# Kernel optimization log

Hardware: AMD Instinct MI355X
Metric: run time of the kernel (lower is better)

## Reference

```python
import jax, jax.numpy as jnp
import numpy as np

ENC_DIM = 128
DEC_DIM = 128
NUM_HEADS = 4
HEAD_DIM = DEC_DIM // NUM_HEADS


def _layernorm(x, g, b, eps=1e-5):
    mu = jnp.mean(x, axis=-1, keepdims=True)
    var = jnp.mean((x - mu) ** 2, axis=-1, keepdims=True)
    return (x - mu) * jax.lax.rsqrt(var + eps) * g + b


def setup_inputs() -> dict:
    key = jax.random.key(0)
    ks = jax.random.split(key, 12)
    B, H, W, D = 2, 16, 16, 16
    s = 0.02
    return {
        "encoder_feat": jax.random.normal(ks[0], (B, ENC_DIM, H, W, D), jnp.float32),
        "decoder_feat": jax.random.normal(ks[1], (B, DEC_DIM, H, W, D), jnp.float32),
        # torch Linear weights stored as [out, in]
        "Wq": jax.random.normal(ks[2], (DEC_DIM, DEC_DIM), jnp.float32) * s,
        "bq": jnp.zeros((DEC_DIM,), jnp.float32),
        "Wk": jax.random.normal(ks[3], (DEC_DIM, ENC_DIM), jnp.float32) * s,
        "bk": jnp.zeros((DEC_DIM,), jnp.float32),
        "Wv": jax.random.normal(ks[4], (DEC_DIM, ENC_DIM), jnp.float32) * s,
        "bv": jnp.zeros((DEC_DIM,), jnp.float32),
        "Wo": jax.random.normal(ks[5], (DEC_DIM, DEC_DIM), jnp.float32) * s,
        "bo": jnp.zeros((DEC_DIM,), jnp.float32),
        "g_enc": jnp.ones((ENC_DIM,), jnp.float32),
        "b_enc": jnp.zeros((ENC_DIM,), jnp.float32),
        "g_dec": jnp.ones((DEC_DIM,), jnp.float32),
        "b_dec": jnp.zeros((DEC_DIM,), jnp.float32),
        "g_out": jnp.ones((DEC_DIM,), jnp.float32),
        "b_out": jnp.zeros((DEC_DIM,), jnp.float32),
        "W1": jax.random.normal(ks[6], (DEC_DIM * 4, DEC_DIM), jnp.float32) * s,
        "b1": jnp.zeros((DEC_DIM * 4,), jnp.float32),
        "W2": jax.random.normal(ks[7], (DEC_DIM, DEC_DIM * 4), jnp.float32) * s,
        "b2": jnp.zeros((DEC_DIM,), jnp.float32),
    }


def reference(encoder_feat, decoder_feat, Wq, bq, Wk, bk, Wv, bv, Wo, bo,
              g_enc, b_enc, g_dec, b_dec, g_out, b_out, W1, b1, W2, b2):
    B, C_dec, H, W_, D = decoder_feat.shape
    N = H * W_ * D
    scale = HEAD_DIM ** -0.5
    # [B, C, H, W, D] -> [B, N, C]
    enc_seq = encoder_feat.reshape(B, -1, N).transpose(0, 2, 1)
    dec_seq = decoder_feat.reshape(B, C_dec, N).transpose(0, 2, 1)
    enc_seq = _layernorm(enc_seq, g_enc, b_enc)
    dec_seq = _layernorm(dec_seq, g_dec, b_dec)
    # projections (torch Linear: x @ W.T + b), split heads -> [B, h, N, d]
    Q = (dec_seq @ Wq.T + bq).reshape(B, N, NUM_HEADS, HEAD_DIM).transpose(0, 2, 1, 3)
    K = (enc_seq @ Wk.T + bk).reshape(B, N, NUM_HEADS, HEAD_DIM).transpose(0, 2, 1, 3)
    V = (enc_seq @ Wv.T + bv).reshape(B, N, NUM_HEADS, HEAD_DIM).transpose(0, 2, 1, 3)
    attn = jnp.einsum('bhqd,bhkd->bhqk', Q, K) * scale  # [B, h, N, N]
    attn = jax.nn.softmax(attn, axis=-1)
    out = jnp.einsum('bhqk,bhkd->bhqd', attn, V)
    out = out.transpose(0, 2, 1, 3).reshape(B, N, C_dec)
    out = out @ Wo.T + bo
    out = dec_seq + out
    h = _layernorm(out, g_out, b_out)
    ffn = jax.nn.gelu(h @ W1.T + b1, approximate=False) @ W2.T + b2
    out = out + ffn
    return out.transpose(0, 2, 1).reshape(B, C_dec, H, W_, D)
```

## Files before the change

kernel.cpp:

```cpp
#include <hip/hip_runtime.h>
#include <hip/hip_bf16.h>
#include <math.h>

#define B_ 2
#define N_ 4096
#define BN_ 8192
#define NH_ 4
#define SPLIT_ 8

using bf16x8   = __attribute__((ext_vector_type(8))) __bf16;
using f32x4    = __attribute__((ext_vector_type(4))) float;
using ushortx8 = __attribute__((ext_vector_type(8))) unsigned short;

#if __has_builtin(__builtin_amdgcn_exp2f)
#define FAST_EXP2(x) __builtin_amdgcn_exp2f(x)
#else
#define FAST_EXP2(x) __expf((x) * 0.6931471805599453f)
#endif

static __device__ __forceinline__ unsigned short f2bf(float f) {
    union { __hip_bfloat16 h; unsigned short u; } c;
    c.h = __float2bfloat16(f);
    return c.u;
}
static __device__ __forceinline__ float bf2f(unsigned short u) {
    union { __hip_bfloat16 h; unsigned short u; } c;
    c.u = u;
    return __bfloat162float(c.h);
}
static __device__ __forceinline__ unsigned int pk2bf(float lo, float hi) {
    return __builtin_amdgcn_perm(__float_as_uint(hi) + 0x8000u,
                                 __float_as_uint(lo) + 0x8000u, 0x07060302u);
}
static __device__ __forceinline__ unsigned int cvtpk(float lo, float hi) {
    unsigned int r;
    asm("v_cvt_pk_bf16_f32 %0, %1, %2" : "=v"(r) : "v"(lo), "v"(hi));
    return r;
}

__global__ __launch_bounds__(256)
void qkv4_kernel(const float* __restrict__ enc, const float* __restrict__ dec,
                 const float* __restrict__ g_enc, const float* __restrict__ b_enc,
                 const float* __restrict__ g_dec, const float* __restrict__ b_dec,
                 const float* __restrict__ Wq, const float* __restrict__ Wk,
                 const float* __restrict__ Wv,
                 const float* __restrict__ bq, const float* __restrict__ bk,
                 const float* __restrict__ bv,
                 const float* __restrict__ Wo, const float* __restrict__ W1,
                 const float* __restrict__ W2,
                 unsigned short* __restrict__ wo, unsigned short* __restrict__ w1,
                 unsigned short* __restrict__ w2,
                 unsigned short* __restrict__ Qh, unsigned short* __restrict__ Kh,
                 unsigned short* __restrict__ Vt,
                 unsigned short* __restrict__ dec_lnb) {
    const int t = threadIdx.x;
    __shared__ float tile[128][33];
    __shared__ float mu_s[32], inv_s[32];
    __shared__ alignas(16) unsigned short Wlds[128][136];
    const int z  = blockIdx.x >> 8;
    const int m0 = (blockIdx.x & 255) * 32;
    const int b  = m0 >> 12, n0 = m0 & 4095;
    const float* inb   = ((z == 0) ? dec : enc) + (size_t)b * 128 * N_;
    const float* gamma = (z == 0) ? g_dec : g_enc;
    const float* beta  = (z == 0) ? b_dec : b_enc;
    const float* Wb    = (z == 0) ? Wq : ((z == 1) ? Wk : Wv);

    if (t < 24) {
        const int e = (int)blockIdx.x * 192 + t * 8;
        const float* src; unsigned short* dst; int off;
        if (e < 16384)       { src = Wo; dst = wo; off = e; }
        else if (e < 81920)  { src = W1; dst = w1; off = e - 16384; }
        else                 { src = W2; dst = w2; off = e - 81920; }
        const float4 a = *(const float4*)(src + off);
        const float4 bq4 = *(const float4*)(src + off + 4);
        uint4 p;
        p.x = pk2bf(a.x, a.y); p.y = pk2bf(a.z, a.w);
        p.z = pk2bf(bq4.x, bq4.y); p.w = pk2bf(bq4.z, bq4.w);
        *(uint4*)(dst + off) = p;
    }

    {
        const int r0 = t >> 3;
        const int cf = (t & 7) * 4;
        #pragma unroll
        for (int j = 0; j < 4; ++j) {
            const int r = r0 + 32 * j;
            const float4 x = *(const float4*)(inb + (size_t)r * N_ + n0 + cf);
            tile[r][cf]     = x.x; tile[r][cf + 1] = x.y;
            tile[r][cf + 2] = x.z; tile[r][cf + 3] = x.w;
        }
    }
    {
        #pragma unroll
        for (int i = 0; i < 8; ++i) {
            const int e   = (i * 256 + t) * 8;
            const int col = e >> 7, k = e & 127;
            const float4 wa = *(const float4*)(Wb + e);
            const float4 wb = *(const float4*)(Wb + e + 4);
            uint4 p;
            p.x = pk2bf(wa.x, wa.y); p.y = pk2bf(wa.z, wa.w);
            p.z = pk2bf(wb.x, wb.y); p.w = pk2bf(wb.z, wb.w);
            *(uint4*)&Wlds[col][k] = p;
        }
    }
    __syncthreads();
    {
        const int tok = t >> 3;
        const int ln  = t & 7;
        float s = 0.f, ss = 0.f;
        for (int c = ln; c < 128; c += 8) {
            const float x = tile[c][tok];
            s += x; ss += x * x;
        }
        for (int m = 1; m < 8; m <<= 1) {
            s  += __shfl_xor(s, m);
            ss += __shfl_xor(ss, m);
        }
        if (ln == 0) {
            const float mu  = s * (1.f / 128.f);
            mu_s[tok]  = mu;
            inv_s[tok] = rsqrtf(ss * (1.f / 128.f) - mu * mu + 1e-5f);
        }
    }
    __syncthreads();

    const int wvx = t >> 6, lane = t & 63;
    const int l15 = lane & 15, quad = lane >> 4;
    const int tokgrp  = (wvx & 1) * 16;
    const int colbase = (wvx >> 1) * 64;
    const bool wrLN   = (z == 0) && ((wvx >> 1) == 0);
    const int tok = tokgrp + l15;
    const float mu  = mu_s[tok];
    const float inv = inv_s[tok];

    bf16x8 af[4];
    #pragma unroll
    for (int kk = 0; kk < 4; ++kk) {
        float y[8];
        #pragma unroll
        for (int j = 0; j < 8; ++j) {
            const int c = kk * 32 + quad * 8 + j;
            y[j] = (tile[c][tok] - mu) * inv * gamma[c] + beta[c];
        }
        union { uint4 u; bf16x8 v8; ushortx8 us; } cvt;
        cvt.u.x = pk2bf(y[0], y[1]); cvt.u.y = pk2bf(y[2], y[3]);
        cvt.u.z = pk2bf(y[4], y[5]); cvt.u.w = pk2bf(y[6], y[7]);
        af[kk] = cvt.v8;
        if (wrLN)
            *(ushortx8*)(dec_lnb + (size_t)(m0 + tok) * 128 + kk * 32 + quad * 8) = cvt.us;
    }

    const float* bias = (z == 0) ? bq : ((z == 1) ? bk : bv);
    const float sc = (z == 0) ? (0.17677669529663687f * 1.4426950408889634f) : 1.f;
    const int nbase = n0 + tokgrp + quad * 4;

    #pragma unroll
    for (int nb = 0; nb < 4; ++nb) {
        const int col = colbase + nb * 16 + l15;
        f32x4 a = {0.f, 0.f, 0.f, 0.f};
        #pragma unroll
        for (int kk = 0; kk < 4; ++kk) {
            const bf16x8 wf = *(const bf16x8*)&Wlds[col][kk * 32 + quad * 8];
            a = __builtin_amdgcn_mfma_f32_16x16x32_bf16(af[kk], wf, a, 0, 0, 0);
        }
        const int h = col >> 5, d = col & 31;
        const float bz = bias[col];
        if (z == 2) {
            ushort4 pk;
            pk.x = f2bf(a[0] + bz);
            pk.y = f2bf(a[1] + bz);
            pk.z = f2bf(a[2] + bz);
            pk.w = f2bf(a[3] + bz);
            *(ushort4*)(Vt + ((size_t)(b * NH_ + h) * 32 + d) * N_ + nbase) = pk;
        } else {
            unsigned short* dst = (z == 0) ? Qh : Kh;
            #pragma unroll
            for (int r = 0; r < 4; ++r)
                dst[((size_t)(b * NH_ + h) * N_ + nbase + r) * 32 + d] = f2bf((a[r] + bz) * sc);
        }
    }
}

__global__ __launch_bounds__(512, 2)
void attn_kernel7(const unsigned short* __restrict__ Qh,
                  const unsigned short* __restrict__ Kh,
                  const unsigned short* __restrict__ Vt,
                  unsigned short* __restrict__ ctx) {
    __shared__ alignas(16) unsigned short sP[8][64][72];
    __shared__ float ldsL[8][64];

    const int gid  = blockIdx.x;
    const int bh   = gid & 7;
    const int qblk = gid >> 3;
    const int t  = threadIdx.x;
    const int wvx = t >> 6, lane = t & 63;
    const int l15 = lane & 15, quad = lane >> 4;
    const int s = wvx;
    const int qw = qblk * 64;
    const size_t hbse = (size_t)bh * N_ * 32;

    bf16x8 qf[4];
    #pragma unroll
    for (int f = 0; f < 4; ++f)
        qf[f] = *(const bf16x8*)(Qh + hbse + (size_t)(qw + f * 16 + l15) * 32 + quad * 8);

    const unsigned short* Kp = Kh + hbse;
    const unsigned short* Vp = Vt + (size_t)bh * 32 * N_;

    bf16x8 ones;
    {
        union { unsigned short u; __bf16 h; } c1; c1.u = 0x3F80;
        #pragma unroll
        for (int j = 0; j < 8; ++j) ones[j] = c1.h;
    }

    f32x4 o0[4], o1[4], lacc[4];
    #pragma unroll
    for (int f = 0; f < 4; ++f) {
        o0[f]   = f32x4{0.f, 0.f, 0.f, 0.f};
        o1[f]   = f32x4{0.f, 0.f, 0.f, 0.f};
        lacc[f] = f32x4{0.f, 0.f, 0.f, 0.f};
    }
    const f32x4 zero = {0.f, 0.f, 0.f, 0.f};

    const int kbeg = s * (N_ / SPLIT_);
    const int kend = kbeg + (N_ / SPLIT_);

    for (int k0 = kbeg; k0 < kend; k0 += 64) {
        bf16x8 kf[4];
        #pragma unroll
        for (int c = 0; c < 4; ++c)
            kf[c] = *(const bf16x8*)(Kp + (size_t)(k0 + c * 16 + l15) * 32 + quad * 8);

        __builtin_amdgcn_s_setprio(1);
        #pragma unroll
        for (int f = 0; f < 4; ++f) {
            #pragma unroll
            for (int c = 0; c < 4; ++c) {
                const f32x4 sv = __builtin_amdgcn_mfma_f32_16x16x32_bf16(kf[c], qf[f], zero, 0, 0, 0);
                const float p0 = FAST_EXP2(sv[0]);
                const float p1 = FAST_EXP2(sv[1]);
                const float p2 = FAST_EXP2(sv[2]);
                const float p3 = FAST_EXP2(sv[3]);
                uint2 pk;
                pk.x = cvtpk(p0, p1);
                pk.y = cvtpk(p2, p3);
                *(uint2*)&sP[wvx][f * 16 + l15][c * 16 + quad * 4] = pk;
            }
        }
        __builtin_amdgcn_s_setprio(0);

        bf16x8 va[2], vb[2];
        #pragma unroll
        for (int s2 = 0; s2 < 2; ++s2) {
            va[s2] = *(const bf16x8*)(Vp + (size_t)l15 * N_        + k0 + s2 * 32 + quad * 8);
            vb[s2] = *(const bf16x8*)(Vp + (size_t)(16 + l15) * N_ + k0 + s2 * 32 + quad * 8);
        }

        __builtin_amdgcn_s_setprio(1);
        #pragma unroll
        for (int f = 0; f < 4; ++f) {
            #pragma unroll
            for (int s2 = 0; s2 < 2; ++s2) {
                const bf16x8 pf = *(const bf16x8*)&sP[wvx][f * 16 + l15][s2 * 32 + quad * 8];
                o0[f]   = __builtin_amdgcn_mfma_f32_16x16x32_bf16(va[s2], pf, o0[f], 0, 0, 0);
                o1[f]   = __builtin_amdgcn_mfma_f32_16x16x32_bf16(vb[s2], pf, o1[f], 0, 0, 0);
                lacc[f] = __builtin_amdgcn_mfma_f32_16x16x32_bf16(ones,   pf, lacc[f], 0, 0, 0);
            }
        }
        __builtin_amdgcn_s_setprio(0);
    }

    __syncthreads();
    float* ldsO = (float*)&sP[0][0][0];
    #pragma unroll
    for (int f = 0; f < 4; ++f) {
        const int q = f * 16 + l15;
        float* row = ldsO + ((size_t)s * 64 + q) * 36;
        *(f32x4*)(row + quad * 4)      = o0[f];
        *(f32x4*)(row + 16 + quad * 4) = o1[f];
        if (quad == 0) ldsL[s][q] = lacc[f][0];
    }
    __syncthreads();

    const int tok = t >> 3;
    const int d0  = (t & 7) * 4;
    f32x4 sum = {0.f, 0.f, 0.f, 0.f};
    float lsum = 0.f;
    #pragma unroll
    for (int w = 0; w < 8; ++w) {
        sum  += *(const f32x4*)(ldsO + ((size_t)w * 64 + tok) * 36 + d0);
        lsum += ldsL[w][tok];
    }
    const float inv = 1.f / lsum;
    uint2 pk;
    pk.x = pk2bf(sum[0] * inv, sum[1] * inv);
    pk.y = pk2bf(sum[2] * inv, sum[3] * inv);
    const int b = bh >> 2, h = bh & 3;
    *(uint2*)(ctx + ((size_t)(b * N_ + qw + tok)) * 128 + h * 32 + d0) = pk;
}

__global__ __launch_bounds__(512)
void fused_tail7_kernel(const unsigned short* __restrict__ ctx,
                        const unsigned short* __restrict__ wo,
                        const float* __restrict__ bo,
                        const unsigned short* __restrict__ decb,
                        const float* __restrict__ g, const float* __restrict__ be,
                        const unsigned short* __restrict__ w1,
                        const float* __restrict__ b1,
                        const unsigned short* __restrict__ w2,
                        const float* __restrict__ b2,
                        float* __restrict__ out) {
    __shared__ float sln[8][2][16];
    __shared__ alignas(16) unsigned short hb_lds[16][136];
    __shared__ alignas(16) unsigned short smid[16][536];
    const int t = threadIdx.x;
    const int wv = t >> 6, lane = t & 63;
    const int l15 = lane & 15, quad = lane >> 4;
    const int m0 = blockIdx.x * 16;
    const int col = wv * 16 + l15;

    bf16x8 af[4];
    #pragma unroll
    for (int kk = 0; kk < 4; ++kk)
        af[kk] = *(const bf16x8*)(ctx + (size_t)(m0 + l15) * 128 + kk * 32 + quad * 8);

    float v[4];
    {
        f32x4 a0 = {0.f, 0.f, 0.f, 0.f};
        f32x4 a1 = {0.f, 0.f, 0.f, 0.f};
        const bf16x8 w0 = *(const bf16x8*)(wo + (size_t)col * 128 + 0 * 32 + quad * 8);
        const bf16x8 w1f = *(const bf16x8*)(wo + (size_t)col * 128 + 1 * 32 + quad * 8);
        const bf16x8 w2f = *(const bf16x8*)(wo + (size_t)col * 128 + 2 * 32 + quad * 8);
        const bf16x8 w3f = *(const bf16x8*)(wo + (size_t)col * 128 + 3 * 32 + quad * 8);
        a0 = __builtin_amdgcn_mfma_f32_16x16x32_bf16(af[0], w0,  a0, 0, 0, 0);
        a1 = __builtin_amdgcn_mfma_f32_16x16x32_bf16(af[1], w1f, a1, 0, 0, 0);
        a0 = __builtin_amdgcn_mfma_f32_16x16x32_bf16(af[2], w2f, a0, 0, 0, 0);
        a1 = __builtin_amdgcn_mfma_f32_16x16x32_bf16(af[3], w3f, a1, 0, 0, 0);
        const f32x4 a = a0 + a1;
        const float bz = bo[col];
        #pragma unroll
        for (int r = 0; r < 4; ++r) {
            const int tok = m0 + quad * 4 + r;
            v[r] = a[r] + bz + bf2f(decb[(size_t)tok * 128 + col]);
        }
    }

    {
        float s[4], ss[4];
        #pragma unroll
        for (int r = 0; r < 4; ++r) {
            float a = v[r];
            float b = v[r] * v[r];
            for (int m = 1; m < 16; m <<= 1) {
                a += __shfl_xor(a, m);
                b += __shfl_xor(b, m);
            }
            s[r] = a; ss[r] = b;
        }
        if (l15 == 0) {
            #pragma unroll
            for (int r = 0; r < 4; ++r) {
                sln[wv][0][quad * 4 + r] = s[r];
                sln[wv][1][quad * 4 + r] = ss[r];
            }
        }
    }
    __syncthreads();

    {
        #pragma unroll
        for (int r = 0; r < 4; ++r) {
            const int tk = quad * 4 + r;
            float stot = 0.f, sstot = 0.f;
            #pragma unroll
            for (int w = 0; w < 8; ++w) {
                stot  += sln[w][0][tk];
                sstot += sln[w][1][tk];
            }
            const float mu  = stot * (1.f / 128.f);
            const float inv = rsqrtf(sstot * (1.f / 128.f) - mu * mu + 1e-5f);
            hb_lds[tk][col] = f2bf((v[r] - mu) * inv * g[col] + be[col]);
        }
    }
    __syncthreads();

    bf16x8 hf[4];
    #pragma unroll
    for (int kk = 0; kk < 4; ++kk)
        hf[kk] = *(const bf16x8*)&hb_lds[l15][kk * 32 + quad * 8];
    #pragma unroll
    for (int nb = 0; nb < 4; ++nb) {
        const int colf = wv * 64 + nb * 16 + l15;
        f32x4 a = {0.f, 0.f, 0.f, 0.f};
        #pragma unroll
        for (int kk = 0; kk < 4; ++kk) {
            const bf16x8 wf = *(const bf16x8*)(w1 + (size_t)colf * 128 + kk * 32 + quad * 8);
            a = __builtin_amdgcn_mfma_f32_16x16x32_bf16(hf[kk], wf, a, 0, 0, 0);
        }
        const float bz = b1[colf];
        #pragma unroll
        for (int r = 0; r < 4; ++r) {
            float x = a[r] + bz;
            x = 0.5f * x * (1.f + erff(x * 0.70710678118f));
            smid[quad * 4 + r][colf] = f2bf(x);
        }
    }
    __syncthreads();

    f32x4 acc0 = {0.f, 0.f, 0.f, 0.f};
    f32x4 acc1 = {0.f, 0.f, 0.f, 0.f};
    #pragma unroll
    for (int kk = 0; kk < 8; ++kk) {
        const bf16x8 afA = *(const bf16x8*)&smid[l15][(2 * kk) * 32 + quad * 8];
        const bf16x8 afB = *(const bf16x8*)&smid[l15][(2 * kk + 1) * 32 + quad * 8];
        const bf16x8 wfA = *(const bf16x8*)(w2 + (size_t)col * 512 + (2 * kk) * 32 + quad * 8);
        const bf16x8 wfB = *(const bf16x8*)(w2 + (size_t)col * 512 + (2 * kk + 1) * 32 + quad * 8);
        acc0 = __builtin_amdgcn_mfma_f32_16x16x32_bf16(afA, wfA, acc0, 0, 0, 0);
        acc1 = __builtin_amdgcn_mfma_f32_16x16x32_bf16(afB, wfB, acc1, 0, 0, 0);
    }

    {
        const int b = m0 >> 12;
        const int nb0 = (m0 & 4095) + quad * 4;
        const float bz = b2[col];
        const f32x4 a = acc0 + acc1;
        f32x4 res;
        #pragma unroll
        for (int r = 0; r < 4; ++r)
            res[r] = a[r] + bz + v[r];
        *(f32x4*)&out[((size_t)(b * 128 + col)) * N_ + nb0] = res;
    }
}

extern "C" void kernel_launch(void* const* d_in, const int* in_sizes, int n_in,
                              void* d_out, int out_size, void* d_ws, size_t ws_size,
                              hipStream_t stream) {
    const float* enc   = (const float*)d_in[0];
    const float* dec   = (const float*)d_in[1];
    const float* Wq    = (const float*)d_in[2];
    const float* bq    = (const float*)d_in[3];
    const float* Wk    = (const float*)d_in[4];
    const float* bk    = (const float*)d_in[5];
    const float* Wv    = (const float*)d_in[6];
    const float* bv    = (const float*)d_in[7];
    const float* Wo    = (const float*)d_in[8];
    const float* bo    = (const float*)d_in[9];
    const float* g_enc = (const float*)d_in[10];
    const float* b_enc = (const float*)d_in[11];
    const float* g_dec = (const float*)d_in[12];
    const float* b_dec = (const float*)d_in[13];
    const float* g_out = (const float*)d_in[14];
    const float* b_out = (const float*)d_in[15];
    const float* W1    = (const float*)d_in[16];
    const float* b1    = (const float*)d_in[17];
    const float* W2    = (const float*)d_in[18];
    const float* b2    = (const float*)d_in[19];
    float* out = (float*)d_out;
    char*  W   = (char*)d_ws;

    unsigned short* wob = (unsigned short*)(W);
    unsigned short* w1b = wob + 16384;
    unsigned short* w2b = w1b + 65536;
    unsigned short* dec_lnb = (unsigned short*)(W + (2560ull << 10));
    unsigned short* Qh      = (unsigned short*)(W + (4608ull << 10));
    unsigned short* Kh      = (unsigned short*)(W + (6656ull << 10));
    unsigned short* Vt      = (unsigned short*)(W + (8704ull << 10));
    unsigned short* ctx     = (unsigned short*)(W + (10752ull << 10));

    qkv4_kernel<<<768, 256, 0, stream>>>(
        enc, dec, g_enc, b_enc, g_dec, b_dec, Wq, Wk, Wv, bq, bk, bv,
        Wo, W1, W2, wob, w1b, w2b, Qh, Kh, Vt, dec_lnb);

    attn_kernel7<<<512, 512, 0, stream>>>(Qh, Kh, Vt, ctx);

    fused_tail7_kernel<<<512, 512, 0, stream>>>(ctx, wob, bo, dec_lnb,
                                                g_out, b_out, w1b, b1, w2b, b2, out);
}
```

Before: 151.1 us.

## Interleave score/exp and PV MFMA halves in attention; prefetch FFN weights; use hw bf16 cvt

The attention inner loop is split into two halves, so the PV MFMAs for the first 32 keys run before the scores and exponentials for the second 32 keys. This lets matrix and transcendental work overlap within a wave. The FFN kernel prefetches the first W1 and W2 weight fragments before the LayerNorm reductions and the barrier, to hide global load latency. The software round-to-bf16 pack is replaced with the hardware v_cvt_pk_bf16_f32 instruction, which may round slightly differently.

```diff
diff --git a/kernel.cpp b/kernel.cpp
--- a/kernel.cpp
+++ b/kernel.cpp
@@ -27,10 +27,6 @@
     union { __hip_bfloat16 h; unsigned short u; } c;
     c.u = u;
     return __bfloat162float(c.h);
-}
-static __device__ __forceinline__ unsigned int pk2bf(float lo, float hi) {
-    return __builtin_amdgcn_perm(__float_as_uint(hi) + 0x8000u,
-                                 __float_as_uint(lo) + 0x8000u, 0x07060302u);
 }
 static __device__ __forceinline__ unsigned int cvtpk(float lo, float hi) {
     unsigned int r;
@@ -74,8 +70,8 @@
         const float4 a = *(const float4*)(src + off);
         const float4 bq4 = *(const float4*)(src + off + 4);
         uint4 p;
-        p.x = pk2bf(a.x, a.y); p.y = pk2bf(a.z, a.w);
-        p.z = pk2bf(bq4.x, bq4.y); p.w = pk2bf(bq4.z, bq4.w);
+        p.x = cvtpk(a.x, a.y); p.y = cvtpk(a.z, a.w);
+        p.z = cvtpk(bq4.x, bq4.y); p.w = cvtpk(bq4.z, bq4.w);
         *(uint4*)(dst + off) = p;
     }
 
@@ -98,8 +94,8 @@
             const float4 wa = *(const float4*)(Wb + e);
             const float4 wb = *(const float4*)(Wb + e + 4);
             uint4 p;
-            p.x = pk2bf(wa.x, wa.y); p.y = pk2bf(wa.z, wa.w);
-            p.z = pk2bf(wb.x, wb.y); p.w = pk2bf(wb.z, wb.w);
+            p.x = cvtpk(wa.x, wa.y); p.y = cvtpk(wa.z, wa.w);
+            p.z = cvtpk(wb.x, wb.y); p.w = cvtpk(wb.z, wb.w);
             *(uint4*)&Wlds[col][k] = p;
         }
     }
@@ -143,8 +139,8 @@
             y[j] = (tile[c][tok] - mu) * inv * gamma[c] + beta[c];
         }
         union { uint4 u; bf16x8 v8; ushortx8 us; } cvt;
-        cvt.u.x = pk2bf(y[0], y[1]); cvt.u.y = pk2bf(y[2], y[3]);
-        cvt.u.z = pk2bf(y[4], y[5]); cvt.u.w = pk2bf(y[6], y[7]);
+        cvt.u.x = cvtpk(y[0], y[1]); cvt.u.y = cvtpk(y[2], y[3]);
+        cvt.u.z = cvtpk(y[4], y[5]); cvt.u.w = cvtpk(y[6], y[7]);
         af[kk] = cvt.v8;
         if (wrLN)
             *(ushortx8*)(dec_lnb + (size_t)(m0 + tok) * 128 + kk * 32 + quad * 8) = cvt.us;
@@ -236,7 +232,7 @@
         #pragma unroll
         for (int f = 0; f < 4; ++f) {
             #pragma unroll
-            for (int c = 0; c < 4; ++c) {
+            for (int c = 0; c < 2; ++c) {
                 const f32x4 sv = __builtin_amdgcn_mfma_f32_16x16x32_bf16(kf[c], qf[f], zero, 0, 0, 0);
                 const float p0 = FAST_EXP2(sv[0]);
                 const float p1 = FAST_EXP2(sv[1]);
@@ -260,13 +256,32 @@
         __builtin_amdgcn_s_setprio(1);
         #pragma unroll
         for (int f = 0; f < 4; ++f) {
+            const bf16x8 pf = *(const bf16x8*)&sP[wvx][f * 16 + l15][quad * 8];
+            o0[f]   = __builtin_amdgcn_mfma_f32_16x16x32_bf16(va[0], pf, o0[f], 0, 0, 0);
+            o1[f]   = __builtin_amdgcn_mfma_f32_16x16x32_bf16(vb[0], pf, o1[f], 0, 0, 0);
+            lacc[f] = __builtin_amdgcn_mfma_f32_16x16x32_bf16(ones,  pf, lacc[f], 0, 0, 0);
+        }
+        #pragma unroll
+        for (int f = 0; f < 4; ++f) {
             #pragma unroll
-            for (int s2 = 0; s2 < 2; ++s2) {
-                const bf16x8 pf = *(const bf16x8*)&sP[wvx][f * 16 + l15][s2 * 32 + quad * 8];
-                o0[f]   = __builtin_amdgcn_mfma_f32_16x16x32_bf16(va[s2], pf, o0[f], 0, 0, 0);
-                o1[f]   = __builtin_amdgcn_mfma_f32_16x16x32_bf16(vb[s2], pf, o1[f], 0, 0, 0);
-                lacc[f] = __builtin_amdgcn_mfma_f32_16x16x32_bf16(ones,   pf, lacc[f], 0, 0, 0);
+            for (int c = 2; c < 4; ++c) {
+                const f32x4 sv = __builtin_amdgcn_mfma_f32_16x16x32_bf16(kf[c], qf[f], zero, 0, 0, 0);
+                const float p0 = FAST_EXP2(sv[0]);
+                const float p1 = FAST_EXP2(sv[1]);
+                const float p2 = FAST_EXP2(sv[2]);
+                const float p3 = FAST_EXP2(sv[3]);
+                uint2 pk;
+                pk.x = cvtpk(p0, p1);
+                pk.y = cvtpk(p2, p3);
+                *(uint2*)&sP[wvx][f * 16 + l15][c * 16 + quad * 4] = pk;
             }
+        }
+        #pragma unroll
+        for (int f = 0; f < 4; ++f) {
+            const bf16x8 pf = *(const bf16x8*)&sP[wvx][f * 16 + l15][32 + quad * 8];
+            o0[f]   = __builtin_amdgcn_mfma_f32_16x16x32_bf16(va[1], pf, o0[f], 0, 0, 0);
+            o1[f]   = __builtin_amdgcn_mfma_f32_16x16x32_bf16(vb[1], pf, o1[f], 0, 0, 0);
+            lacc[f] = __builtin_amdgcn_mfma_f32_16x16x32_bf16(ones,  pf, lacc[f], 0, 0, 0);
         }
         __builtin_amdgcn_s_setprio(0);
     }
@@ -294,8 +309,8 @@
     }
     const float inv = 1.f / lsum;
     uint2 pk;
-    pk.x = pk2bf(sum[0] * inv, sum[1] * inv);
-    pk.y = pk2bf(sum[2] * inv, sum[3] * inv);
+    pk.x = cvtpk(sum[0] * inv, sum[1] * inv);
+    pk.y = cvtpk(sum[2] * inv, sum[3] * inv);
     const int b = bh >> 2, h = bh & 3;
     *(uint2*)(ctx + ((size_t)(b * N_ + qw + tok)) * 128 + h * 32 + d0) = pk;
 }
@@ -346,6 +361,14 @@
         }
     }
 
+    bf16x8 w1p[4];
+    {
+        const int colf = wv * 64 + l15;
+        #pragma unroll
+        for (int kk = 0; kk < 4; ++kk)
+            w1p[kk] = *(const bf16x8*)(w1 + (size_t)colf * 128 + kk * 32 + quad * 8);
+    }
+
     {
         float s[4], ss[4];
         #pragma unroll
@@ -395,7 +418,8 @@
         f32x4 a = {0.f, 0.f, 0.f, 0.f};
         #pragma unroll
         for (int kk = 0; kk < 4; ++kk) {
-            const bf16x8 wf = *(const bf16x8*)(w1 + (size_t)colf * 128 + kk * 32 + quad * 8);
+            const bf16x8 wf = (nb == 0) ? w1p[kk]
+                : *(const bf16x8*)(w1 + (size_t)colf * 128 + kk * 32 + quad * 8);
             a = __builtin_amdgcn_mfma_f32_16x16x32_bf16(hf[kk], wf, a, 0, 0, 0);
         }
         const float bz = b1[colf];
@@ -406,6 +430,9 @@
             smid[quad * 4 + r][colf] = f2bf(x);
         }
     }
+
+    bf16x8 w2pA = *(const bf16x8*)(w2 + (size_t)col * 512 + 0 * 32 + quad * 8);
+    bf16x8 w2pB = *(const bf16x8*)(w2 + (size_t)col * 512 + 1 * 32 + quad * 8);
     __syncthreads();
 
     f32x4 acc0 = {0.f, 0.f, 0.f, 0.f};
@@ -414,8 +441,10 @@
     for (int kk = 0; kk < 8; ++kk) {
         const bf16x8 afA = *(const bf16x8*)&smid[l15][(2 * kk) * 32 + quad * 8];
         const bf16x8 afB = *(const bf16x8*)&smid[l15][(2 * kk + 1) * 32 + quad * 8];
-        const bf16x8 wfA = *(const bf16x8*)(w2 + (size_t)col * 512 + (2 * kk) * 32 + quad * 8);
-        const bf16x8 wfB = *(const bf16x8*)(w2 + (size_t)col * 512 + (2 * kk + 1) * 32 + quad * 8);
+        const bf16x8 wfA = (kk == 0) ? w2pA
+            : *(const bf16x8*)(w2 + (size_t)col * 512 + (2 * kk) * 32 + quad * 8);
+        const bf16x8 wfB = (kk == 0) ? w2pB
+            : *(const bf16x8*)(w2 + (size_t)col * 512 + (2 * kk + 1) * 32 + quad * 8);
         acc0 = __builtin_amdgcn_mfma_f32_16x16x32_bf16(afA, wfA, acc0, 0, 0, 0);
         acc1 = __builtin_amdgcn_mfma_f32_16x16x32_bf16(afB, wfB, acc1, 0, 0, 0);
     }
```

New measurement: 150.3 us. No clear change (-0.5%).
